# Kernel tuning notes

Measured on AMD Instinct MI355X. Metric: run time of the kernel, lower is better.

Reference implementation:

```python
import jax, jax.numpy as jnp
import numpy as np

BOS_ID = 0
EOS_ID = 1


def setup_inputs() -> dict:
    key = jax.random.key(0)
    ks = jax.random.split(key, 16)
    B, L, F = 64, 200, 512
    H, E, A = 512, 512, 512
    V, T = 50257, 21
    D = E + F  # rnn input_dim
    s = lambda n: 1.0 / np.sqrt(n)
    ref = jax.random.randint(ks[0], (B, T), 2, V, dtype=jnp.int32)
    ref = ref.at[:, 0].set(BOS_ID).at[:, -1].set(EOS_ID)
    return {
        "encoder_output": jax.random.normal(ks[1], (B, L, F), jnp.float32),
        "decoder_init_hidden": jax.random.normal(ks[2], (1, B, H), jnp.float32),
        "encoding_mask": jnp.ones((B, L, 1), jnp.float32),
        "temp_seg": jax.random.uniform(ks[3], (B, 2), jnp.float32),
        "embed_table": jax.random.normal(ks[4], (V, E), jnp.float32) * 0.02,
        "W_ih": jax.random.normal(ks[5], (3 * H, D), jnp.float32) * s(D),
        "W_hh": jax.random.normal(ks[6], (3 * H, H), jnp.float32) * s(H),
        "b_ih": jnp.zeros((3 * H,), jnp.float32),
        "b_hh": jnp.zeros((3 * H,), jnp.float32),
        "Wa_enc": jax.random.normal(ks[7], (F, A), jnp.float32) * s(F),
        "Wa_h": jax.random.normal(ks[8], (H, A), jnp.float32) * s(H),
        "v_att": jax.random.normal(ks[9], (A,), jnp.float32) * s(A),
        "W_out": jax.random.normal(ks[10], (V, H), jnp.float32) * s(H),
        "b_out": jnp.zeros((V,), jnp.float32),
        "ref_caption": ref,
    }


def reference(encoder_output, decoder_init_hidden, encoding_mask, temp_seg,
              embed_table, W_ih, W_hh, b_ih, b_hh,
              Wa_enc, Wa_h, v_att, W_out, b_out, ref_caption):
    # Teacher-forced training forward of RNNSeqDecoder (GRU, 1 layer).
    B, T = ref_caption.shape
    V = embed_table.shape[0]
    enc_proj = jnp.einsum('blf,fa->bla', encoder_output, Wa_enc)  # precompute attn enc term
    mask = encoding_mask[..., 0]  # (B,L)
    h0 = decoder_init_hidden[0]   # (B,H)

    def step(h, word):
        emb = embed_table[word]                                        # (B,E)
        # additive attention over encoder states (masked)
        score = jnp.einsum('bla,a->bl', jnp.tanh(enc_proj + (h @ Wa_h)[:, None, :]), v_att)
        score = jnp.where(mask > 0, score, -1e9)
        attn = jax.nn.softmax(score, axis=1)
        ctx = jnp.einsum('bl,blf->bf', attn, encoder_output)           # (B,F)
        x = jnp.concatenate([emb, ctx], axis=1)                        # (B,E+F)
        # PyTorch GRU cell
        gi = x @ W_ih.T + b_ih
        gh = h @ W_hh.T + b_hh
        i_r, i_z, i_n = jnp.split(gi, 3, axis=1)
        h_r, h_z, h_n = jnp.split(gh, 3, axis=1)
        r = jax.nn.sigmoid(i_r + h_r)
        z = jax.nn.sigmoid(i_z + h_z)
        n = jnp.tanh(i_n + r * h_n)
        h_new = (1.0 - z) * n + z * h
        logp = jax.nn.log_softmax(h_new @ W_out.T + b_out, axis=1)     # (B,V)
        return h_new, logp

    _, logps = jax.lax.scan(step, h0, ref_caption[:, :-1].T)           # (T-1,B,V)
    first = jnp.zeros((B, 1, V), logps.dtype)  # BOS_ID == 0, matches torch.zeros(...) + BOS_ID
    caption_prob = jnp.concatenate([first, jnp.swapaxes(logps, 0, 1)], axis=1)  # (B,T,V)
    return caption_prob
```

## Files before the change

kernel.cpp:

```cpp
#include <hip/hip_runtime.h>
#include <stdint.h>
#include <stddef.h>

#define B_ 64
#define L_ 200
#define F_ 512
#define H_ 512
#define A_ 512
#define E_ 512
#define V_ 50257
#define PADV 50304
#define T_ 21
#define D_ 1024
#define NBLK_LOG 786
#define BH (B_ * H_)
#define BD (B_ * D_)
#define NROW 1280

typedef __attribute__((ext_vector_type(8))) short short8;
typedef __attribute__((ext_vector_type(4))) float f32x4;

__device__ __forceinline__ unsigned short f2b(float f) {
  unsigned int u = __builtin_bit_cast(unsigned int, f);
  u += 0x7FFFu + ((u >> 16) & 1u);
  return (unsigned short)(u >> 16);
}
__device__ __forceinline__ float b2f(unsigned short s) {
  unsigned int u = ((unsigned int)s) << 16;
  return __builtin_bit_cast(float, u);
}
__device__ __forceinline__ f32x4 mfma16(short8 a, short8 b, f32x4 c) {
  return __builtin_amdgcn_mfma_f32_16x16x32_bf16(a, b, c, 0, 0, 0);
}
__device__ __forceinline__ int hsoff(int b, int j) {
  return (((b >> 4) * 16 + (j >> 5)) * 64 + (((j >> 3) & 3) * 16 + (b & 15))) * 8 + (j & 7);
}
__device__ __forceinline__ int xoff(int b, int k) {
  return (((b >> 4) * 32 + (k >> 5)) * 64 + (((k >> 3) & 3) * 16 + (b & 15))) * 8 + (k & 7);
}


__global__ void k_cvt(const float* __restrict__ src, unsigned short* __restrict__ dst, int n4) {
  int i = blockIdx.x * blockDim.x + threadIdx.x;
  int stride = gridDim.x * blockDim.x;
  const float4* s4 = (const float4*)src;
  ushort4* d4 = (ushort4*)dst;
  for (; i < n4; i += stride) {
    float4 v = s4[i];
    ushort4 o;
    o.x = f2b(v.x); o.y = f2b(v.y); o.z = f2b(v.z); o.w = f2b(v.w);
    d4[i] = o;
  }
}

__global__ void k_wfrag(const float* __restrict__ src, unsigned short* __restrict__ dst, int K) {
  int rt = blockIdx.x;
  int r15 = threadIdx.x & 15;
  int row = rt * 16 + r15;
  int nch = K >> 3;
  int kpw = K >> 5;
  for (int kc = threadIdx.x >> 4; kc < nch; kc += 16) {
    const float4* s = (const float4*)(src + (size_t)row * K + kc * 8);
    float4 x = s[0], y = s[1];
    short8 o;
    o[0] = f2b(x.x); o[1] = f2b(x.y); o[2] = f2b(x.z); o[3] = f2b(x.w);
    o[4] = f2b(y.x); o[5] = f2b(y.y); o[6] = f2b(y.z); o[7] = f2b(y.w);
    *(short8*)(dst + ((size_t)(rt * kpw + (kc >> 2)) * 64 + ((kc & 3) * 16 + r15)) * 8) = o;
  }
}

__global__ void k_transcvt(const float* __restrict__ src, unsigned short* __restrict__ dst, int R, int C) {
  __shared__ float tile[64][65];
  int cb = blockIdx.x * 64, rb = blockIdx.y * 64;
  int tx = threadIdx.x & 63, ty = threadIdx.x >> 6;
#pragma unroll
  for (int i = 0; i < 16; ++i) {
    int r = ty * 16 + i;
    tile[r][tx] = src[(size_t)(rb + r) * C + cb + tx];
  }
  __syncthreads();
#pragma unroll
  for (int i = 0; i < 16; ++i) {
    int c = ty * 16 + i;
    dst[(size_t)(cb + c) * R + rb + tx] = f2b(tile[tx][c]);
  }
}

__global__ void k_trans32(const float* __restrict__ src, float* __restrict__ dst, int R, int C) {
  __shared__ float tile[64][65];
  int cb = blockIdx.x * 64, rb = blockIdx.y * 64;
  int tx = threadIdx.x & 63, ty = threadIdx.x >> 6;
#pragma unroll
  for (int i = 0; i < 16; ++i) {
    int r = ty * 16 + i;
    tile[r][tx] = src[(size_t)(rb + r) * C + cb + tx];
  }
  __syncthreads();
#pragma unroll
  for (int i = 0; i < 16; ++i) {
    int c = ty * 16 + i;
    dst[(size_t)(cb + c) * R + rb + tx] = tile[tx][c];
  }
}

__global__ void k_hs0(const float* __restrict__ src, unsigned short* __restrict__ hs) {
  int b = blockIdx.x;
  for (int j = threadIdx.x; j < H_; j += 256)
    hs[hsoff(b, j)] = f2b(src[(size_t)b * H_ + j]);
}

__global__ void k_embAll(const int* __restrict__ ref, const float* __restrict__ et,
                         unsigned short* __restrict__ xAll) {
  int b = blockIdx.x, tp = blockIdx.y;
  int word = ref[b * T_ + tp];
  const float* er = et + (size_t)word * E_;
  unsigned short* dst = xAll + (size_t)tp * BD;
  int c = threadIdx.x;
  const float4* s = (const float4*)(er + c * 8);
  float4 x = s[0], y = s[1];
  short8 o;
  o[0] = f2b(x.x); o[1] = f2b(x.y); o[2] = f2b(x.z); o[3] = f2b(x.w);
  o[4] = f2b(y.x); o[5] = f2b(y.y); o[6] = f2b(y.z); o[7] = f2b(y.w);
  *(short8*)(dst + xoff(b, c * 8)) = o;
}

__global__ __launch_bounds__(256, 2) void k_encproj2(const unsigned short* __restrict__ encb,
                                                     const unsigned short* __restrict__ WaTb,
                                                     unsigned short* __restrict__ epb) {
  __shared__ unsigned short al[32768];
  int tid = threadIdx.x;
  size_t rowbase = (size_t)blockIdx.x * 64;
  for (int idx = tid; idx < 4096; idx += 256) {
    int row = idx >> 6, seg = idx & 63;
    unsigned char* dp = (unsigned char*)al + row * 1024 + ((seg * 16) ^ ((row & 7) << 4));
    *(short8*)dp = *(const short8*)(encb + (rowbase + row) * F_ + seg * 8);
  }
  __syncthreads();
  int w = tid >> 6, lane = tid & 63, ln15 = lane & 15, g = lane >> 4;
  int sw = (ln15 & 7) << 4;
  const unsigned char* alb = (const unsigned char*)al;
  int mrow = w * 16 + ln15;
  for (int nt = 0; nt < 32; ++nt) {
    f32x4 acc = {0.f, 0.f, 0.f, 0.f};
    const unsigned short* brow = WaTb + (size_t)(nt * 16 + ln15) * F_ + 8 * g;
#pragma unroll 4
    for (int kk = 0; kk < 16; ++kk) {
      short8 bf = *(const short8*)(brow + kk * 32);
      short8 af = *(const short8*)(alb + mrow * 1024 + ((kk * 64 + 16 * g) ^ sw));
      acc = mfma16(af, bf, acc);
    }
#pragma unroll
    for (int r = 0; r < 4; ++r) {
      size_t m = rowbase + w * 16 + 4 * g + r;
      epb[m * A_ + nt * 16 + ln15] = f2b(acc[r]);
    }
  }
}

__global__ void k_zero0(float* __restrict__ out) {
  int b = blockIdx.y;
  float* o = out + (size_t)b * T_ * V_;
  int v0 = blockIdx.x * 1024 + threadIdx.x;
#pragma unroll
  for (int i = 0; i < 4; ++i) { int v = v0 + i * 256; if (v < V_) o[v] = 0.f; }
}


__global__ __launch_bounds__(256) void k_hwgh(const unsigned short* __restrict__ Wahf,
                                              const unsigned short* __restrict__ Wfhh,
                                              const unsigned short* __restrict__ hs,
                                              float* __restrict__ hw,
                                              float* __restrict__ ghG) {
  int blk = blockIdx.x;
  int w = threadIdx.x >> 6, lane = threadIdx.x & 63;
  int ln15 = lane & 15, g = lane >> 4;
  if (blk < 32) {
    f32x4 acc = {0.f, 0.f, 0.f, 0.f};
#pragma unroll 4
    for (int kk = 0; kk < 16; ++kk) {
      short8 av = *(const short8*)(Wahf + (((size_t)blk * 16 + kk) * 64 + lane) * 8);
      short8 hv = *(const short8*)(hs + (((size_t)w * 16 + kk) * 64 + lane) * 8);
      acc = mfma16(av, hv, acc);
    }
#pragma unroll
    for (int r = 0; r < 4; ++r) {
      int a = blk * 16 + 4 * g + r;
      int b = w * 16 + ln15;
      hw[(size_t)b * 512 + a] = acc[r];
    }
  } else {
    int base = (blk - 32) * 3;
#pragma unroll
    for (int i = 0; i < 3; ++i) {
      int jt = base + i;
      f32x4 acc = {0.f, 0.f, 0.f, 0.f};
#pragma unroll
      for (int kk = 0; kk < 16; ++kk) {
        short8 wv = *(const short8*)(Wfhh + (((size_t)jt * 16 + kk) * 64 + lane) * 8);
        short8 hv = *(const short8*)(hs + (((size_t)w * 16 + kk) * 64 + lane) * 8);
        acc = mfma16(wv, hv, acc);
      }
#pragma unroll
      for (int r = 0; r < 4; ++r) {
        int j = jt * 16 + 4 * g + r;
        int b = w * 16 + ln15;
        ghG[(size_t)j * B_ + b] = acc[r];
      }
    }
  }
}


__global__ __launch_bounds__(1024) void k_attB(const float* __restrict__ mask,
                                               const float* __restrict__ vatt,
                                               const unsigned short* __restrict__ encb,
                                               const unsigned short* __restrict__ epb,
                                               const float* __restrict__ hw,
                                               unsigned short* __restrict__ xplane) {
  __shared__ float sm[208];
  __shared__ float ctxp[16][F_];
  __shared__ float ctxF[F_];
  int b = blockIdx.x;
  int tid = threadIdx.x;
  int w = tid >> 6, lane = tid & 63;
  float hwv[8], vv[8];
  {
    const float4* hp = (const float4*)(hw + (size_t)b * 512 + lane * 8);
    const float4* vp = (const float4*)(vatt + lane * 8);
    float4 h0 = hp[0], h1 = hp[1], v0 = vp[0], v1 = vp[1];
    hwv[0] = h0.x; hwv[1] = h0.y; hwv[2] = h0.z; hwv[3] = h0.w;
    hwv[4] = h1.x; hwv[5] = h1.y; hwv[6] = h1.z; hwv[7] = h1.w;
    vv[0] = v0.x; vv[1] = v0.y; vv[2] = v0.z; vv[3] = v0.w;
    vv[4] = v1.x; vv[5] = v1.y; vv[6] = v1.z; vv[7] = v1.w;
  }
  for (int l = w; l < L_; l += 16) {
    short8 ev = *(const short8*)(epb + ((size_t)(b * L_ + l)) * 512 + lane * 8);
    float p = 0.f;
#pragma unroll
    for (int j = 0; j < 8; ++j) {
      float x = b2f((unsigned short)ev[j]) + hwv[j];
      float e2 = __expf(x + x);
      p = fmaf(1.f - 2.f / (e2 + 1.f), vv[j], p);
    }
    for (int o = 1; o < 64; o <<= 1) p += __shfl_xor(p, o);
    if (lane == 0) {
      float mk = mask[b * L_ + l];
      sm[l] = (mk > 0.f) ? p : -1e9f;
    }
  }
  __syncthreads();
  if (tid < 64) {
    float m = -1e30f;
    for (int l = tid; l < L_; l += 64) m = fmaxf(m, sm[l]);
    for (int o = 1; o < 64; o <<= 1) m = fmaxf(m, __shfl_xor(m, o));
    float s = 0.f;
    for (int l = tid; l < L_; l += 64) s += __expf(sm[l] - m);
    for (int o = 1; o < 64; o <<= 1) s += __shfl_xor(s, o);
    float inv = 1.f / s;
    for (int l = tid; l < L_; l += 64) sm[l] = __expf(sm[l] - m) * inv;
  }
  __syncthreads();
  float c[8] = {0.f, 0.f, 0.f, 0.f, 0.f, 0.f, 0.f, 0.f};
  for (int l = w; l < L_; l += 16) {
    float wgt = sm[l];
    short8 ev = *(const short8*)(encb + ((size_t)(b * L_ + l)) * 512 + lane * 8);
#pragma unroll
    for (int j = 0; j < 8; ++j) c[j] = fmaf(wgt, b2f((unsigned short)ev[j]), c[j]);
  }
#pragma unroll
  for (int j = 0; j < 8; ++j) ctxp[w][lane * 8 + j] = c[j];
  __syncthreads();
  if (tid < 512) {
    float s = 0.f;
#pragma unroll
    for (int q = 0; q < 16; ++q) s += ctxp[q][tid];
    ctxF[tid] = s;
  }
  __syncthreads();
  if (tid < 64) {
    short8 o;
#pragma unroll
    for (int j = 0; j < 8; ++j) o[j] = f2b(ctxF[tid * 8 + j]);
    *(short8*)(xplane + xoff(b, E_ + tid * 8)) = o;
  }
}


__global__ __launch_bounds__(256) void k_stepB(const unsigned short* __restrict__ Wfih,
                                               const float* __restrict__ bih,
                                               const float* __restrict__ bhh,
                                               const unsigned short* __restrict__ xplane,
                                               const float* __restrict__ ghG,
                                               const float* __restrict__ hBold,
                                               unsigned short* __restrict__ hsnew,
                                               float* __restrict__ hBnew) {
  int bx = blockIdx.x;
  int w = threadIdx.x >> 6, lane = threadIdx.x & 63;
  int ln15 = lane & 15, g = lane >> 4;
  f32x4 z4 = {0.f, 0.f, 0.f, 0.f};
  f32x4 aIr = z4, aIz = z4, aIn = z4;
#pragma unroll 2
  for (int kk = 0; kk < 32; ++kk) {
    short8 xv = *(const short8*)(xplane + (((size_t)w * 32 + kk) * 64 + lane) * 8);
    aIr = mfma16(*(const short8*)(Wfih + (((size_t)(0 * 32 + bx) * 32 + kk) * 64 + lane) * 8), xv, aIr);
    aIz = mfma16(*(const short8*)(Wfih + (((size_t)(32 + bx) * 32 + kk) * 64 + lane) * 8), xv, aIz);
    aIn = mfma16(*(const short8*)(Wfih + (((size_t)(64 + bx) * 32 + kk) * 64 + lane) * 8), xv, aIn);
  }
  int jb = bx * 16;
#pragma unroll
  for (int r = 0; r < 4; ++r) {
    int j = jb + 4 * g + r;
    int b = w * 16 + ln15;
    float ir = aIr[r] + bih[j];
    float iz = aIz[r] + bih[512 + j];
    float in_ = aIn[r] + bih[1024 + j];
    float hrv = ghG[(size_t)j * B_ + b] + bhh[j];
    float hzv = ghG[(size_t)(512 + j) * B_ + b] + bhh[512 + j];
    float hnv = ghG[(size_t)(1024 + j) * B_ + b] + bhh[1024 + j];
    float rg = 1.f / (1.f + __expf(-(ir + hrv)));
    float zg = 1.f / (1.f + __expf(-(iz + hzv)));
    float e2 = __expf(2.f * (in_ + rg * hnv));
    float ng = 1.f - 2.f / (e2 + 1.f);
    float ho = hBold[(size_t)b * H_ + j];
    float hv = (1.f - zg) * ng + zg * ho;
    hBnew[(size_t)b * H_ + j] = hv;
    hsnew[hsoff(b, j)] = f2b(hv);
  }
}


__global__ __launch_bounds__(512) void k_blog(const unsigned short* __restrict__ Wb,
                                              const float* __restrict__ bout,
                                              const unsigned short* __restrict__ hsAll,
                                              float* __restrict__ pm, float* __restrict__ ps,
                                              float* __restrict__ out,
                                              unsigned short* __restrict__ lws, int mode) {
  __shared__ float tile[64][68];
  __shared__ float redm[64][8], reds[64][8];
  int tid = threadIdx.x;
  int w = tid >> 6, lane = tid & 63, ln15 = lane & 15, g = lane >> 4;
  int vt = w & 3, mh = w >> 2;
  int vcol = blockIdx.x * 64 + vt * 16 + ln15;
  bool vok = vcol < V_;
  int vr = vok ? vcol : (V_ - 1);
  const unsigned short* brow = Wb + (size_t)vr * H_ + 8 * g;
  short8 wb[16];
#pragma unroll
  for (int kk = 0; kk < 16; ++kk) wb[kk] = *(const short8*)(brow + kk * 32);
  float bo = bout[vr];
  int row = tid >> 3, s8 = tid & 7;

  for (int t = 0; t < T_ - 1; ++t) {
    const unsigned short* hp = hsAll + (size_t)(t + 1) * BH;
#pragma unroll
    for (int mp = 0; mp < 2; ++mp) {
      int mt = mh * 2 + mp;
      f32x4 acc = {0.f, 0.f, 0.f, 0.f};
#pragma unroll
      for (int kk = 0; kk < 16; ++kk) {
        short8 a0 = *(const short8*)(hp + (((size_t)(mt * 16 + kk)) * 64 + lane) * 8);
        acc = mfma16(a0, wb[kk], acc);
      }
#pragma unroll
      for (int r = 0; r < 4; ++r) {
        int bi = mt * 16 + 4 * g + r;
        tile[bi][vt * 16 + ln15] = vok ? acc[r] + bo : -1e30f;
      }
    }
    __syncthreads();
    float v[8];
#pragma unroll
    for (int q = 0; q < 2; ++q) {
      float4 fv = *(const float4*)&tile[row][s8 * 8 + q * 4];
      v[q * 4 + 0] = fv.x; v[q * 4 + 1] = fv.y; v[q * 4 + 2] = fv.z; v[q * 4 + 3] = fv.w;
    }
    int cb = blockIdx.x * 64 + s8 * 8;
    if (mode == 1) {
      unsigned short* orow = lws + ((size_t)t * 64 + row) * PADV + cb;
      short8 o0;
#pragma unroll
      for (int i = 0; i < 8; ++i) o0[i] = f2b(v[i]);
      *(short8*)orow = o0;
    } else {
      float* orow = out + ((size_t)row * T_ + (t + 1)) * V_ + cb;
      if (cb + 8 <= V_) {
#pragma unroll
        for (int i = 0; i < 8; ++i) orow[i] = v[i];
      } else {
        for (int i = 0; i < 8; ++i)
          if (cb + i < V_) orow[i] = v[i];
      }
    }
    float m = -1e30f;
#pragma unroll
    for (int i = 0; i < 8; ++i) m = fmaxf(m, v[i]);
    float s = 0.f;
#pragma unroll
    for (int i = 0; i < 8; ++i) s += __expf(v[i] - m);
    redm[row][s8] = m; reds[row][s8] = s;
    __syncthreads();
    if (s8 == 0) {
      float m4 = -1e30f;
#pragma unroll
      for (int i = 0; i < 8; ++i) m4 = fmaxf(m4, redm[row][i]);
      float s4 = 0.f;
#pragma unroll
      for (int i = 0; i < 8; ++i) s4 += reds[row][i] * __expf(redm[row][i] - m4);
      size_t rho = (size_t)t * 64 + row;
      pm[rho * NBLK_LOG + blockIdx.x] = m4;
      ps[rho * NBLK_LOG + blockIdx.x] = s4;
    }
    __syncthreads();
  }
}

__global__ __launch_bounds__(256) void k_lse(const float* __restrict__ pm,
                                             const float* __restrict__ ps,
                                             float* __restrict__ lse) {
  int rho = blockIdx.x;
  int tid = threadIdx.x;
  float m = -1e30f, s = 0.f;
  for (int p = tid; p < NBLK_LOG; p += 256) {
    float pmv = pm[(size_t)rho * NBLK_LOG + p], psv = ps[(size_t)rho * NBLK_LOG + p];
    float nm = fmaxf(m, pmv);
    s = s * __expf(m - nm) + psv * __expf(pmv - nm);
    m = nm;
  }
  __shared__ float lm[256], ls[256];
  lm[tid] = m; ls[tid] = s;
  __syncthreads();
  for (int o = 128; o > 0; o >>= 1) {
    if (tid < o) {
      float m2 = lm[tid + o], s2 = ls[tid + o];
      float nm = fmaxf(lm[tid], m2);
      ls[tid] = ls[tid] * __expf(lm[tid] - nm) + s2 * __expf(m2 - nm);
      lm[tid] = nm;
    }
    __syncthreads();
  }
  if (tid == 0) lse[rho] = lm[0] + logf(ls[0]);
}

__global__ __launch_bounds__(256) void k_fin(float* __restrict__ out, const float* __restrict__ lse) {
  int rho = blockIdx.x;
  int tp = rho >> 6, b = rho & 63;
  float Lv = lse[rho];
  float* o = out + ((size_t)b * T_ + (tp + 1)) * V_;
  int tid = threadIdx.x;
  for (int i = tid; i < 12564; i += 256) {
    float4* o4 = (float4*)o;
    float4 v = o4[i];
    v.x -= Lv; v.y -= Lv; v.z -= Lv; v.w -= Lv;
    o4[i] = v;
  }
  if (tid == 0) o[50256] -= Lv;
}

__global__ __launch_bounds__(256) void k_finb(const unsigned short* __restrict__ lws,
                                              const float* __restrict__ lse,
                                              float* __restrict__ out) {
  int rho = blockIdx.x >> 1;
  int half = blockIdx.x & 1;
  int tp = rho >> 6, b = rho & 63;
  float Lv = lse[rho];
  const unsigned short* src = lws + (size_t)(tp * 64 + b) * PADV;
  float* o = out + ((size_t)b * T_ + (tp + 1)) * V_;
  int tid = threadIdx.x;
  int i0 = half * 3141, i1 = i0 + 3141;
  for (int i = i0 + tid; i < i1; i += 256) {
    short8 sv = *(const short8*)(src + i * 8);
    float4 v0, v1;
    v0.x = b2f((unsigned short)sv[0]) - Lv; v0.y = b2f((unsigned short)sv[1]) - Lv;
    v0.z = b2f((unsigned short)sv[2]) - Lv; v0.w = b2f((unsigned short)sv[3]) - Lv;
    v1.x = b2f((unsigned short)sv[4]) - Lv; v1.y = b2f((unsigned short)sv[5]) - Lv;
    v1.z = b2f((unsigned short)sv[6]) - Lv; v1.w = b2f((unsigned short)sv[7]) - Lv;
    *(float4*)(o + i * 8) = v0;
    *(float4*)(o + i * 8 + 4) = v1;
  }
  if (half == 1 && tid == 0) o[50256] = b2f(src[50256]) - Lv;
}


extern "C" void kernel_launch(void* const* d_in, const int* in_sizes, int n_in,
                              void* d_out, int out_size, void* d_ws, size_t ws_size,
                              hipStream_t stream) {
  const float* enc   = (const float*)d_in[0];
  const float* dih   = (const float*)d_in[1];
  const float* mask  = (const float*)d_in[2];
  const float* et    = (const float*)d_in[4];
  const float* Wih   = (const float*)d_in[5];
  const float* Whh   = (const float*)d_in[6];
  const float* bih   = (const float*)d_in[7];
  const float* bhh   = (const float*)d_in[8];
  const float* Waenc = (const float*)d_in[9];
  const float* Wah   = (const float*)d_in[10];
  const float* vatt  = (const float*)d_in[11];
  const float* Wout  = (const float*)d_in[12];
  const float* bout  = (const float*)d_in[13];
  const int*   ref   = (const int*)d_in[14];
  float* out = (float*)d_out;

  char* w = (char*)d_ws;
  size_t o = 0;
  unsigned short* Wb    = (unsigned short*)(w + o); o += (size_t)V_ * H_ * 2;
  unsigned short* Wfih  = (unsigned short*)(w + o); o += (size_t)1536 * 1024 * 2;
  unsigned short* Wfhh  = (unsigned short*)(w + o); o += (size_t)1536 * 512 * 2;
  unsigned short* WaTb  = (unsigned short*)(w + o); o += (size_t)512 * 512 * 2;
  unsigned short* Wahf  = (unsigned short*)(w + o); o += (size_t)512 * 512 * 2;
  float* WahT32 = (float*)(w + o); o += (size_t)512 * 512 * 4;
  unsigned short* encb  = (unsigned short*)(w + o); o += (size_t)B_ * L_ * F_ * 2;
  unsigned short* epb   = (unsigned short*)(w + o); o += (size_t)B_ * L_ * A_ * 2;
  unsigned short* xAll  = (unsigned short*)(w + o); o += (size_t)20 * BD * 2;
  unsigned short* hsAll = (unsigned short*)(w + o); o += (size_t)T_ * BH * 2;
  float* hBAll = (float*)(w + o); o += (size_t)T_ * BH * 4;
  float* ghG   = (float*)(w + o); o += (size_t)1536 * B_ * 4;
  float* hw    = (float*)(w + o); o += (size_t)B_ * A_ * 4;
  float* pm  = (float*)(w + o); o += (size_t)NROW * NBLK_LOG * 4;
  float* ps  = (float*)(w + o); o += (size_t)NROW * NBLK_LOG * 4;
  float* lse = (float*)(w + o); o += (size_t)NROW * 4 + 256;
  unsigned short* lws = (unsigned short*)(w + o);
  size_t need = o + (size_t)NROW * PADV * 2;
  int mode = (ws_size >= need) ? 1 : 0;

  k_cvt<<<4096, 256, 0, stream>>>(Wout, Wb, V_ * H_ / 4);
  k_cvt<<<2048, 256, 0, stream>>>(enc, encb, B_ * L_ * F_ / 4);
  k_wfrag<<<96, 256, 0, stream>>>(Wih, Wfih, 1024);
  k_wfrag<<<96, 256, 0, stream>>>(Whh, Wfhh, 512);
  k_transcvt<<<dim3(8, 8), 256, 0, stream>>>(Waenc, WaTb, 512, 512);
  k_trans32<<<dim3(8, 8), 256, 0, stream>>>(Wah, WahT32, 512, 512);
  k_wfrag<<<32, 256, 0, stream>>>(WahT32, Wahf, 512);
  k_hs0<<<64, 256, 0, stream>>>(dih, hsAll);
  k_embAll<<<dim3(64, 20), 64, 0, stream>>>(ref, et, xAll);
  k_encproj2<<<200, 256, 0, stream>>>(encb, WaTb, epb);
  k_zero0<<<dim3(50, 64), 256, 0, stream>>>(out);

  for (int t = 0; t < T_ - 1; ++t) {
    const float* hB_t = (t == 0) ? dih : (hBAll + (size_t)t * BH);
    float* hB_n = hBAll + (size_t)(t + 1) * BH;
    const unsigned short* hs_t = hsAll + (size_t)t * BH;
    unsigned short* hs_n = hsAll + (size_t)(t + 1) * BH;
    unsigned short* xp = xAll + (size_t)t * BD;
    k_hwgh<<<64, 256, 0, stream>>>(Wahf, Wfhh, hs_t, hw, ghG);
    k_attB<<<64, 1024, 0, stream>>>(mask, vatt, encb, epb, hw, xp);
    k_stepB<<<32, 256, 0, stream>>>(Wfih, bih, bhh, xp, ghG, hB_t, hs_n, hB_n);
  }
  k_blog<<<NBLK_LOG, 512, 0, stream>>>(Wb, bout, hsAll, pm, ps, out, lws, mode);
  k_lse<<<1280, 256, 0, stream>>>(pm, ps, lse);
  if (mode == 1) k_finb<<<2560, 256, 0, stream>>>(lws, lse, out);
  else k_fin<<<1280, 256, 0, stream>>>(out, lse);
}
```

Measured before the change: 1.504 ms.

## Move logsumexp out of logits GEMM into fused lse+finalize kernel

The output-projection kernel no longer computes per-block max/sum partials. It now uses 256 threads, each wave computing two M-tiles at once, and double-buffers the shared tile so one barrier per step suffices. A new fused kernel reads each bf16 logit row, computes the logsumexp, and writes the normalized fp32 output in one pass. This drops the separate lse kernel and the partial-stat buffers, and the fallback path gets the same fused treatment. The cost is that the final kernel now reads the bf16 row twice per block instead of once.

After: 1.362 ms. 9.4% less time.

```diff
diff --git a/kernel.cpp b/kernel.cpp
--- a/kernel.cpp
+++ b/kernel.cpp
@@ -329,18 +329,15 @@
 }
 
 
-__global__ __launch_bounds__(512) void k_blog(const unsigned short* __restrict__ Wb,
+__global__ __launch_bounds__(256) void k_blog(const unsigned short* __restrict__ Wb,
                                               const float* __restrict__ bout,
                                               const unsigned short* __restrict__ hsAll,
-                                              float* __restrict__ pm, float* __restrict__ ps,
                                               float* __restrict__ out,
                                               unsigned short* __restrict__ lws, int mode) {
-  __shared__ float tile[64][68];
-  __shared__ float redm[64][8], reds[64][8];
+  __shared__ float tile[2][64][68];
   int tid = threadIdx.x;
   int w = tid >> 6, lane = tid & 63, ln15 = lane & 15, g = lane >> 4;
-  int vt = w & 3, mh = w >> 2;
-  int vcol = blockIdx.x * 64 + vt * 16 + ln15;
+  int vcol = blockIdx.x * 64 + w * 16 + ln15;
   bool vok = vcol < V_;
   int vr = vok ? vcol : (V_ - 1);
   const unsigned short* brow = Wb + (size_t)vr * H_ + 8 * g;
@@ -348,126 +345,97 @@
 #pragma unroll
   for (int kk = 0; kk < 16; ++kk) wb[kk] = *(const short8*)(brow + kk * 32);
   float bo = bout[vr];
-  int row = tid >> 3, s8 = tid & 7;
+  int row = tid >> 2, seg = tid & 3;
 
   for (int t = 0; t < T_ - 1; ++t) {
     const unsigned short* hp = hsAll + (size_t)(t + 1) * BH;
+    int buf = t & 1;
 #pragma unroll
     for (int mp = 0; mp < 2; ++mp) {
-      int mt = mh * 2 + mp;
-      f32x4 acc = {0.f, 0.f, 0.f, 0.f};
+      f32x4 z4 = {0.f, 0.f, 0.f, 0.f};
+      f32x4 acc0 = z4, acc1 = z4;
 #pragma unroll
       for (int kk = 0; kk < 16; ++kk) {
-        short8 a0 = *(const short8*)(hp + (((size_t)(mt * 16 + kk)) * 64 + lane) * 8);
-        acc = mfma16(a0, wb[kk], acc);
+        short8 a0 = *(const short8*)(hp + (((mp * 2 + 0) * 16 + kk) * 64 + lane) * 8);
+        short8 a1 = *(const short8*)(hp + (((mp * 2 + 1) * 16 + kk) * 64 + lane) * 8);
+        acc0 = mfma16(a0, wb[kk], acc0);
+        acc1 = mfma16(a1, wb[kk], acc1);
       }
 #pragma unroll
       for (int r = 0; r < 4; ++r) {
-        int bi = mt * 16 + 4 * g + r;
-        tile[bi][vt * 16 + ln15] = vok ? acc[r] + bo : -1e30f;
+        int bi0 = (mp * 2 + 0) * 16 + 4 * g + r;
+        int bi1 = (mp * 2 + 1) * 16 + 4 * g + r;
+        tile[buf][bi0][w * 16 + ln15] = vok ? acc0[r] + bo : -1e30f;
+        tile[buf][bi1][w * 16 + ln15] = vok ? acc1[r] + bo : -1e30f;
       }
     }
     __syncthreads();
-    float v[8];
-#pragma unroll
-    for (int q = 0; q < 2; ++q) {
-      float4 fv = *(const float4*)&tile[row][s8 * 8 + q * 4];
+    float v[16];
+#pragma unroll
+    for (int q = 0; q < 4; ++q) {
+      float4 fv = *(const float4*)&tile[buf][row][seg * 16 + q * 4];
       v[q * 4 + 0] = fv.x; v[q * 4 + 1] = fv.y; v[q * 4 + 2] = fv.z; v[q * 4 + 3] = fv.w;
     }
-    int cb = blockIdx.x * 64 + s8 * 8;
+    int cb = blockIdx.x * 64 + seg * 16;
     if (mode == 1) {
       unsigned short* orow = lws + ((size_t)t * 64 + row) * PADV + cb;
-      short8 o0;
-#pragma unroll
-      for (int i = 0; i < 8; ++i) o0[i] = f2b(v[i]);
+      short8 o0, o1;
+#pragma unroll
+      for (int i = 0; i < 8; ++i) { o0[i] = f2b(v[i]); o1[i] = f2b(v[8 + i]); }
       *(short8*)orow = o0;
+      *(short8*)(orow + 8) = o1;
     } else {
       float* orow = out + ((size_t)row * T_ + (t + 1)) * V_ + cb;
-      if (cb + 8 <= V_) {
-#pragma unroll
-        for (int i = 0; i < 8; ++i) orow[i] = v[i];
+      if (cb + 16 <= V_) {
+#pragma unroll
+        for (int q = 0; q < 4; ++q)
+          *(float4*)(orow + q * 4) = make_float4(v[q * 4], v[q * 4 + 1], v[q * 4 + 2], v[q * 4 + 3]);
       } else {
-        for (int i = 0; i < 8; ++i)
+        for (int i = 0; i < 16; ++i)
           if (cb + i < V_) orow[i] = v[i];
       }
     }
-    float m = -1e30f;
-#pragma unroll
-    for (int i = 0; i < 8; ++i) m = fmaxf(m, v[i]);
-    float s = 0.f;
-#pragma unroll
-    for (int i = 0; i < 8; ++i) s += __expf(v[i] - m);
-    redm[row][s8] = m; reds[row][s8] = s;
-    __syncthreads();
-    if (s8 == 0) {
-      float m4 = -1e30f;
-#pragma unroll
-      for (int i = 0; i < 8; ++i) m4 = fmaxf(m4, redm[row][i]);
-      float s4 = 0.f;
-#pragma unroll
-      for (int i = 0; i < 8; ++i) s4 += reds[row][i] * __expf(redm[row][i] - m4);
-      size_t rho = (size_t)t * 64 + row;
-      pm[rho * NBLK_LOG + blockIdx.x] = m4;
-      ps[rho * NBLK_LOG + blockIdx.x] = s4;
-    }
-    __syncthreads();
-  }
-}
-
-__global__ __launch_bounds__(256) void k_lse(const float* __restrict__ pm,
-                                             const float* __restrict__ ps,
-                                             float* __restrict__ lse) {
+  }
+}
+
+__global__ __launch_bounds__(256) void k_lsefin(const unsigned short* __restrict__ lws,
+                                                float* __restrict__ out) {
+  __shared__ float lm[256], ls[256];
+  __shared__ float lvs;
   int rho = blockIdx.x;
+  int tp = rho >> 6, b = rho & 63;
+  const unsigned short* src = lws + (size_t)(tp * 64 + b) * PADV;
+  float* o = out + ((size_t)b * T_ + (tp + 1)) * V_;
   int tid = threadIdx.x;
   float m = -1e30f, s = 0.f;
-  for (int p = tid; p < NBLK_LOG; p += 256) {
-    float pmv = pm[(size_t)rho * NBLK_LOG + p], psv = ps[(size_t)rho * NBLK_LOG + p];
-    float nm = fmaxf(m, pmv);
-    s = s * __expf(m - nm) + psv * __expf(pmv - nm);
+  for (int i = tid; i < PADV / 8; i += 256) {
+    short8 sv = *(const short8*)(src + i * 8);
+    float x0 = b2f((unsigned short)sv[0]), x1 = b2f((unsigned short)sv[1]);
+    float x2 = b2f((unsigned short)sv[2]), x3 = b2f((unsigned short)sv[3]);
+    float x4 = b2f((unsigned short)sv[4]), x5 = b2f((unsigned short)sv[5]);
+    float x6 = b2f((unsigned short)sv[6]), x7 = b2f((unsigned short)sv[7]);
+    float cm = fmaxf(fmaxf(fmaxf(x0, x1), fmaxf(x2, x3)), fmaxf(fmaxf(x4, x5), fmaxf(x6, x7)));
+    float cs = __expf(x0 - cm) + __expf(x1 - cm) + __expf(x2 - cm) + __expf(x3 - cm) +
+               __expf(x4 - cm) + __expf(x5 - cm) + __expf(x6 - cm) + __expf(x7 - cm);
+    float nm = fmaxf(m, cm);
+    s = s * __expf(m - nm) + cs * __expf(cm - nm);
     m = nm;
   }
-  __shared__ float lm[256], ls[256];
   lm[tid] = m; ls[tid] = s;
   __syncthreads();
-  for (int o = 128; o > 0; o >>= 1) {
-    if (tid < o) {
-      float m2 = lm[tid + o], s2 = ls[tid + o];
+  for (int o2 = 128; o2 > 0; o2 >>= 1) {
+    if (tid < o2) {
+      float m2 = lm[tid + o2], s2 = ls[tid + o2];
       float nm = fmaxf(lm[tid], m2);
       ls[tid] = ls[tid] * __expf(lm[tid] - nm) + s2 * __expf(m2 - nm);
       lm[tid] = nm;
     }
     __syncthreads();
   }
-  if (tid == 0) lse[rho] = lm[0] + logf(ls[0]);
-}
-
-__global__ __launch_bounds__(256) void k_fin(float* __restrict__ out, const float* __restrict__ lse) {
-  int rho = blockIdx.x;
-  int tp = rho >> 6, b = rho & 63;
-  float Lv = lse[rho];
-  float* o = out + ((size_t)b * T_ + (tp + 1)) * V_;
-  int tid = threadIdx.x;
-  for (int i = tid; i < 12564; i += 256) {
-    float4* o4 = (float4*)o;
-    float4 v = o4[i];
-    v.x -= Lv; v.y -= Lv; v.z -= Lv; v.w -= Lv;
-    o4[i] = v;
-  }
-  if (tid == 0) o[50256] -= Lv;
-}
-
-__global__ __launch_bounds__(256) void k_finb(const unsigned short* __restrict__ lws,
-                                              const float* __restrict__ lse,
-                                              float* __restrict__ out) {
-  int rho = blockIdx.x >> 1;
-  int half = blockIdx.x & 1;
-  int tp = rho >> 6, b = rho & 63;
-  float Lv = lse[rho];
-  const unsigned short* src = lws + (size_t)(tp * 64 + b) * PADV;
-  float* o = out + ((size_t)b * T_ + (tp + 1)) * V_;
-  int tid = threadIdx.x;
-  int i0 = half * 3141, i1 = i0 + 3141;
-  for (int i = i0 + tid; i < i1; i += 256) {
+  if (tid == 0) lvs = lm[0] + logf(ls[0]);
+  __syncthreads();
+  float Lv = lvs;
+  for (int i = tid; i < 6282; i += 256) {
     short8 sv = *(const short8*)(src + i * 8);
     float4 v0, v1;
     v0.x = b2f((unsigned short)sv[0]) - Lv; v0.y = b2f((unsigned short)sv[1]) - Lv;
@@ -477,7 +445,38 @@
     *(float4*)(o + i * 8) = v0;
     *(float4*)(o + i * 8 + 4) = v1;
   }
-  if (half == 1 && tid == 0) o[50256] = b2f(src[50256]) - Lv;
+  if (tid == 0) o[50256] = b2f(src[50256]) - Lv;
+}
+
+__global__ __launch_bounds__(256) void k_lsefin0(float* __restrict__ out) {
+  __shared__ float lm[256], ls[256];
+  __shared__ float lvs;
+  int rho = blockIdx.x;
+  int tp = rho >> 6, b = rho & 63;
+  float* o = out + ((size_t)b * T_ + (tp + 1)) * V_;
+  int tid = threadIdx.x;
+  float m = -1e30f, s = 0.f;
+  for (int v = tid; v < V_; v += 256) {
+    float x = o[v];
+    float nm = fmaxf(m, x);
+    s = s * __expf(m - nm) + __expf(x - nm);
+    m = nm;
+  }
+  lm[tid] = m; ls[tid] = s;
+  __syncthreads();
+  for (int o2 = 128; o2 > 0; o2 >>= 1) {
+    if (tid < o2) {
+      float m2 = lm[tid + o2], s2 = ls[tid + o2];
+      float nm = fmaxf(lm[tid], m2);
+      ls[tid] = ls[tid] * __expf(lm[tid] - nm) + s2 * __expf(m2 - nm);
+      lm[tid] = nm;
+    }
+    __syncthreads();
+  }
+  if (tid == 0) lvs = lm[0] + logf(ls[0]);
+  __syncthreads();
+  float Lv = lvs;
+  for (int v = tid; v < V_; v += 256) o[v] -= Lv;
 }
 
 
@@ -514,10 +513,7 @@
   unsigned short* hsAll = (unsigned short*)(w + o); o += (size_t)T_ * BH * 2;
   float* hBAll = (float*)(w + o); o += (size_t)T_ * BH * 4;
   float* ghG   = (float*)(w + o); o += (size_t)1536 * B_ * 4;
-  float* hw    = (float*)(w + o); o += (size_t)B_ * A_ * 4;
-  float* pm  = (float*)(w + o); o += (size_t)NROW * NBLK_LOG * 4;
-  float* ps  = (float*)(w + o); o += (size_t)NROW * NBLK_LOG * 4;
-  float* lse = (float*)(w + o); o += (size_t)NROW * 4 + 256;
+  float* hw    = (float*)(w + o); o += (size_t)B_ * A_ * 4 + 256;
   unsigned short* lws = (unsigned short*)(w + o);
   size_t need = o + (size_t)NROW * PADV * 2;
   int mode = (ws_size >= need) ? 1 : 0;
@@ -544,8 +540,7 @@
     k_attB<<<64, 1024, 0, stream>>>(mask, vatt, encb, epb, hw, xp);
     k_stepB<<<32, 256, 0, stream>>>(Wfih, bih, bhh, xp, ghG, hB_t, hs_n, hB_n);
   }
-  k_blog<<<NBLK_LOG, 512, 0, stream>>>(Wb, bout, hsAll, pm, ps, out, lws, mode);
-  k_lse<<<1280, 256, 0, stream>>>(pm, ps, lse);
-  if (mode == 1) k_finb<<<2560, 256, 0, stream>>>(lws, lse, out);
-  else k_fin<<<1280, 256, 0, stream>>>(out, lse);
-}
+  k_blog<<<NBLK_LOG, 256, 0, stream>>>(Wb, bout, hsAll, out, lws, mode);
+  if (mode == 1) k_lsefin<<<1280, 256, 0, stream>>>(lws, out);
+  else k_lsefin0<<<1280, 256, 0, stream>>>(out);
+}
```
